# Performance work log

Hardware: AMD Instinct MI355X
Metric: run time of the kernel (lower is better)

Reference implementation:

```python
import jax, jax.numpy as jnp
import numpy as np

N_TOKENS = 4096
EMBED = 1024
ATTN = 64


def setup_inputs() -> dict:
    key = jax.random.key(0)
    k1, k2, k3, k4 = jax.random.split(key, 4)
    tokens = jax.random.normal(k1, (N_TOKENS, EMBED), dtype=jnp.float32)
    mask = jnp.ones((1, N_TOKENS), dtype=jnp.float32)
    W_Q = jax.random.uniform(k2, (EMBED, ATTN), dtype=jnp.float32)
    W_K = jax.random.uniform(k3, (EMBED, ATTN), dtype=jnp.float32)
    W_V = jax.random.uniform(k4, (EMBED, ATTN), dtype=jnp.float32)
    return {"tokens": tokens, "mask": mask, "W_Q": W_Q, "W_K": W_K, "W_V": W_V}


def reference(tokens, mask, W_Q, W_K, W_V):
    # Q, K, V: (n_tokens, attn)
    Q = tokens @ W_Q
    K = tokens @ W_K
    V = tokens @ W_V
    scale = jnp.sqrt(jnp.asarray(ATTN, dtype=tokens.dtype))
    # scores: (n_tokens, n_tokens); multiplicative mask then scale, as in source
    scores = (Q @ K.T) * mask
    attn = jax.nn.softmax(scores / scale, axis=1)
    return attn @ V
```

## Files before the change

kernel.cpp:

```cpp
#include <hip/hip_runtime.h>
#include <math.h>

#define NT 4096
#define EMB 1024
#define DH 64
#define PLANE (NT * DH)
#define NSPLIT 16
#define KPS (NT / NSPLIT)
#define KVB 128
#define KSPLIT 8
#define LOG2E 1.44269504088896f

typedef __attribute__((ext_vector_type(8))) short short8;
typedef __attribute__((ext_vector_type(16))) float f32x16;
typedef unsigned short u16;

union U8 { short8 s; uint4 u; unsigned short h[8]; unsigned int w[4]; };

static __device__ __forceinline__ unsigned short f2bf(float x) {
    union { float f; unsigned int u; } v; v.f = x;
    unsigned int r = v.u + 0x7fffu + ((v.u >> 16) & 1u);
    return (unsigned short)(r >> 16);
}
static __device__ __forceinline__ float bf2f(unsigned short h) {
    union { unsigned int u; float f; } v; v.u = ((unsigned int)h) << 16;
    return v.f;
}
static __device__ __forceinline__ unsigned int cvtpk(float a, float b) {
    unsigned int r;
    asm("v_cvt_pk_bf16_f32 %0, %1, %2" : "=v"(r) : "v"(a), "v"(b));
    return r;
}
static __device__ __forceinline__ void split2(float a, float b,
                                              unsigned int& h, unsigned int& lo) {
    h = cvtpk(a, b);
    union { unsigned int u; float f; } ua, ub;
    ua.u = h << 16;
    ub.u = h & 0xffff0000u;
    lo = cvtpk(a - ua.f, b - ub.f);
}

__global__ __launch_bounds__(256) void proj_mfma(
    const float* __restrict__ tokens,
    const float* __restrict__ wq, const float* __restrict__ wk,
    const float* __restrict__ wv,
    float* __restrict__ part)
{
    __shared__ u16 Th[128][64];
    __shared__ u16 Tl[128][64];
    __shared__ u16 Wh[96][64];
    __shared__ u16 Wl[96][64];

    const int t  = threadIdx.x;
    const int rb = blockIdx.x;
    const int cb = blockIdx.y;
    const int ks = blockIdx.z;
    const int w    = t >> 6;
    const int lane = t & 63;
    const int g    = lane >> 5;
    const int c    = lane & 31;
    const int rowbase = rb * 128;

    f32x16 acc[3];
#pragma unroll
    for (int ct = 0; ct < 3; ++ct)
#pragma unroll
        for (int i = 0; i < 16; ++i) acc[ct][i] = 0.f;

    for (int st = 0; st < 2; ++st) {
        const int kbase = ks * (EMB / KSPLIT) + st * 64;
        __syncthreads();
#pragma unroll
        for (int i = 0; i < 4; ++i) {
            int idx = t + 256 * i;
            int r = idx >> 3;
            int slot = idx & 7;
            const float* gp = tokens + (size_t)(rowbase + r) * EMB + kbase + slot * 8;
            float4 a = *(const float4*)gp;
            float4 b = *(const float4*)(gp + 4);
            uint4 H, L;
            split2(a.x, a.y, H.x, L.x);
            split2(a.z, a.w, H.y, L.y);
            split2(b.x, b.y, H.z, L.z);
            split2(b.z, b.w, H.w, L.w);
            int dst = (slot ^ (r & 7)) * 8;
            *(uint4*)&Th[r][dst] = H;
            *(uint4*)&Tl[r][dst] = L;
        }
#pragma unroll
        for (int i = 0; i < 3; ++i) {
            int idx = t + 256 * i;
            int col = idx >> 3;
            int slot = idx & 7;
            int colg = cb * 96 + col;
            const float* W = (colg < 64) ? wq : (colg < 128) ? wk : wv;
            const float* wp = W + (size_t)(kbase + slot * 8) * DH + (colg & 63);
            float x[8];
#pragma unroll
            for (int j = 0; j < 8; ++j) x[j] = wp[j * DH];
            uint4 H, L;
            split2(x[0], x[1], H.x, L.x);
            split2(x[2], x[3], H.y, L.y);
            split2(x[4], x[5], H.z, L.z);
            split2(x[6], x[7], H.w, L.w);
            int dst = (slot ^ (col & 7)) * 8;
            *(uint4*)&Wh[col][dst] = H;
            *(uint4*)&Wl[col][dst] = L;
        }
        __syncthreads();

#pragma unroll
        for (int kt = 0; kt < 4; ++kt) {
            int sA = kt * 2 + g;
            int offA = ((sA ^ (c & 7)) * 8);
            short8 ah = *(const short8*)&Th[w * 32 + c][offA];
            short8 al = *(const short8*)&Tl[w * 32 + c][offA];
#pragma unroll
            for (int ct = 0; ct < 3; ++ct) {
                short8 bh = *(const short8*)&Wh[ct * 32 + c][offA];
                short8 bl = *(const short8*)&Wl[ct * 32 + c][offA];
                acc[ct] = __builtin_amdgcn_mfma_f32_32x32x16_bf16(ah, bh, acc[ct], 0, 0, 0);
                acc[ct] = __builtin_amdgcn_mfma_f32_32x32x16_bf16(ah, bl, acc[ct], 0, 0, 0);
                acc[ct] = __builtin_amdgcn_mfma_f32_32x32x16_bf16(al, bh, acc[ct], 0, 0, 0);
            }
        }
    }

#pragma unroll
    for (int ct = 0; ct < 3; ++ct)
#pragma unroll
        for (int r = 0; r < 16; ++r) {
            int row_l = (r & 3) + 8 * (r >> 2) + 4 * g;
            part[((size_t)ks * NT + rowbase + w * 32 + row_l) * 192 + cb * 96 + ct * 32 + c]
                = acc[ct][r];
        }
}

__global__ __launch_bounds__(256) void merge_conv(
    const float* __restrict__ part, const float* __restrict__ mask,
    u16* __restrict__ Qhg, u16* __restrict__ Qlg,
    u16* __restrict__ Khg, u16* __restrict__ Klg, u16* __restrict__ Vbg)
{
    int tid = blockIdx.x * 256 + threadIdx.x;
    int row = tid / 24;
    int c8  = tid % 24;
    int colbase = c8 * 8;

    float v[8];
#pragma unroll
    for (int i = 0; i < 8; ++i) v[i] = 0.f;
#pragma unroll
    for (int s = 0; s < KSPLIT; ++s) {
        const float* p = part + ((size_t)s * NT + row) * 192 + colbase;
        float4 a = *(const float4*)p;
        float4 b = *(const float4*)(p + 4);
        v[0] += a.x; v[1] += a.y; v[2] += a.z; v[3] += a.w;
        v[4] += b.x; v[5] += b.y; v[6] += b.z; v[7] += b.w;
    }

    int plane = colbase >> 6;
    int pc = colbase & 63;
    size_t o = (size_t)row * DH + pc;
    if (plane == 0) {
        uint4 H, L;
        split2(v[0], v[1], H.x, L.x);
        split2(v[2], v[3], H.y, L.y);
        split2(v[4], v[5], H.z, L.z);
        split2(v[6], v[7], H.w, L.w);
        *(uint4*)&Qhg[o] = H;
        *(uint4*)&Qlg[o] = L;
    } else if (plane == 1) {
        float mk = mask[row] * 0.125f * LOG2E;
        uint4 H, L;
        split2(v[0] * mk, v[1] * mk, H.x, L.x);
        split2(v[2] * mk, v[3] * mk, H.y, L.y);
        split2(v[4] * mk, v[5] * mk, H.z, L.z);
        split2(v[6] * mk, v[7] * mk, H.w, L.w);
        *(uint4*)&Khg[o] = H;
        *(uint4*)&Klg[o] = L;
    } else {
        uint4 H;
        H.x = cvtpk(v[0], v[1]);
        H.y = cvtpk(v[2], v[3]);
        H.z = cvtpk(v[4], v[5]);
        H.w = cvtpk(v[6], v[7]);
        *(uint4*)&Vbg[o] = H;
    }
}

__global__ __launch_bounds__(256, 2) void attn_mfma(
    const u16* __restrict__ Qhg, const u16* __restrict__ Qlg,
    const u16* __restrict__ Khg, const u16* __restrict__ Klg,
    const u16* __restrict__ Vbg,
    u16* __restrict__ opart, float* __restrict__ mlbuf)
{
    __shared__ u16 Kh[128][64];
    __shared__ u16 Kl[128][64];
    __shared__ unsigned int V2[64][64];

    const int t    = threadIdx.x;
    const int qb   = blockIdx.x;
    const int sp   = blockIdx.y;
    const int wq   = t >> 6;
    const int lane = t & 63;
    const int g    = lane >> 5;
    const int c    = lane & 31;
    const int qrow = qb * 128 + wq * 32 + c;

    short8 qh[4], ql[4];
#pragma unroll
    for (int kt = 0; kt < 4; ++kt) {
        size_t o = (size_t)qrow * DH + kt * 16 + g * 8;
        U8 H, L;
        H.u = *(const uint4*)&Qhg[o];
        L.u = *(const uint4*)&Qlg[o];
        qh[kt] = H.s;
        ql[kt] = L.s;
    }

    f32x16 oa[2];
#pragma unroll
    for (int i = 0; i < 16; ++i) { oa[0][i] = 0.f; oa[1][i] = 0.f; }
    float m = -INFINITY, l = 0.f;

    for (int cb = 0; cb < KPS / KVB; ++cb) {
        const int kv = sp * KPS + cb * KVB;
        __syncthreads();
#pragma unroll
        for (int it = 0; it < 4; ++it) {
            int idx = it * 256 + t;
            int j = idx >> 3, gr = idx & 7;
            int colp = (gr * 8) ^ ((j & 7) * 8);
            *(uint4*)&Kh[j][colp] = *(const uint4*)&Khg[(size_t)(kv + j) * DH + gr * 8];
            *(uint4*)&Kl[j][colp] = *(const uint4*)&Klg[(size_t)(kv + j) * DH + gr * 8];
        }
#pragma unroll
        for (int it = 0; it < 2; ++it) {
            int idx = it * 256 + t;
            int a2 = idx >> 3, dg = idx & 7;
            uint4 r0 = *(const uint4*)&Vbg[(size_t)(kv + a2 * 2) * DH + dg * 8];
            uint4 r1 = *(const uint4*)&Vbg[(size_t)(kv + a2 * 2 + 1) * DH + dg * 8];
            const unsigned int* p0 = (const unsigned int*)&r0;
            const unsigned int* p1 = (const unsigned int*)&r1;
            unsigned int wv_[8];
#pragma unroll
            for (int i = 0; i < 4; ++i) {
                wv_[2 * i]     = (p0[i] & 0xFFFFu) | (p1[i] << 16);
                wv_[2 * i + 1] = (p0[i] >> 16)     | (p1[i] & 0xFFFF0000u);
            }
            int colp = (dg * 8) ^ ((a2 & 7) * 8);
            *(uint4*)&V2[a2][colp]     = *(uint4*)&wv_[0];
            *(uint4*)&V2[a2][colp + 4] = *(uint4*)&wv_[4];
        }
        __syncthreads();

        f32x16 st[4];
#pragma unroll
        for (int jt = 0; jt < 4; ++jt)
#pragma unroll
            for (int i = 0; i < 16; ++i) st[jt][i] = 0.f;
#pragma unroll
        for (int kt = 0; kt < 4; ++kt) {
            int colp = ((kt * 2 + g) * 8) ^ ((c & 7) * 8);
#pragma unroll
            for (int jt = 0; jt < 4; ++jt) {
                short8 kh = *(const short8*)&Kh[jt * 32 + c][colp];
                short8 kl = *(const short8*)&Kl[jt * 32 + c][colp];
                st[jt] = __builtin_amdgcn_mfma_f32_32x32x16_bf16(kh, qh[kt], st[jt], 0, 0, 0);
                st[jt] = __builtin_amdgcn_mfma_f32_32x32x16_bf16(kh, ql[kt], st[jt], 0, 0, 0);
                st[jt] = __builtin_amdgcn_mfma_f32_32x32x16_bf16(kl, qh[kt], st[jt], 0, 0, 0);
            }
        }

        float p[64];
        float pm = -INFINITY;
#pragma unroll
        for (int jt = 0; jt < 4; ++jt)
#pragma unroll
            for (int r = 0; r < 16; ++r) pm = fmaxf(pm, st[jt][r]);
        pm = fmaxf(pm, __shfl_xor(pm, 32));
        float mn = fmaxf(m, pm);
        float f  = exp2f(m - mn);
        float rs = 0.f;
#pragma unroll
        for (int jt = 0; jt < 4; ++jt)
#pragma unroll
            for (int r = 0; r < 16; ++r) {
                p[jt * 16 + r] = exp2f(st[jt][r] - mn);
                rs += p[jt * 16 + r];
            }
        rs += __shfl_xor(rs, 32);
        l = l * f + rs;
        m = mn;

        short8 pa[8];
#pragma unroll
        for (int jt = 0; jt < 4; ++jt) {
            const float* pp = &p[jt * 16];
            unsigned int A1 = cvtpk(pp[0], pp[1]),   B1 = cvtpk(pp[4], pp[5]);
            unsigned int A2 = cvtpk(pp[2], pp[3]),   B2 = cvtpk(pp[6], pp[7]);
            unsigned int A3 = cvtpk(pp[8], pp[9]),   B3 = cvtpk(pp[12], pp[13]);
            unsigned int A4 = cvtpk(pp[10], pp[11]), B4 = cvtpk(pp[14], pp[15]);
            unsigned int xA1 = (unsigned int)__shfl_xor((int)A1, 32);
            unsigned int xB1 = (unsigned int)__shfl_xor((int)B1, 32);
            unsigned int xA2 = (unsigned int)__shfl_xor((int)A2, 32);
            unsigned int xB2 = (unsigned int)__shfl_xor((int)B2, 32);
            unsigned int xA3 = (unsigned int)__shfl_xor((int)A3, 32);
            unsigned int xB3 = (unsigned int)__shfl_xor((int)B3, 32);
            unsigned int xA4 = (unsigned int)__shfl_xor((int)A4, 32);
            unsigned int xB4 = (unsigned int)__shfl_xor((int)B4, 32);
            U8 f0, f1;
            f0.w[0] = g ? xB1 : A1;
            f0.w[1] = g ? xB2 : A2;
            f0.w[2] = g ? B1  : xA1;
            f0.w[3] = g ? B2  : xA2;
            f1.w[0] = g ? xB3 : A3;
            f1.w[1] = g ? xB4 : A4;
            f1.w[2] = g ? B3  : xA3;
            f1.w[3] = g ? B4  : xA4;
            pa[jt * 2]     = f0.s;
            pa[jt * 2 + 1] = f1.s;
        }

#pragma unroll
        for (int r = 0; r < 16; ++r) {
            float fr = __shfl(f, (r & 3) + 8 * (r >> 2) + 4 * g);
            oa[0][r] *= fr;
            oa[1][r] *= fr;
        }

#pragma unroll
        for (int dt = 0; dt < 2; ++dt) {
#pragma unroll
            for (int ksl = 0; ksl < 8; ++ksl) {
                U8 bf;
#pragma unroll
                for (int pq = 0; pq < 4; ++pq) {
                    int j2 = ksl * 8 + g * 4 + pq;
                    int col = (dt * 32 + c) ^ ((j2 & 7) * 8);
                    bf.w[pq] = V2[j2][col];
                }
                oa[dt] = __builtin_amdgcn_mfma_f32_32x32x16_bf16(pa[ksl], bf.s, oa[dt], 0, 0, 0);
            }
        }
    }

    float inv = 1.f / l;
#pragma unroll
    for (int r = 0; r < 16; ++r) {
        int crow = (r & 3) + 8 * (r >> 2) + 4 * g;
        float li = __shfl(inv, crow);
        int row = qb * 128 + wq * 32 + crow;
        size_t o = ((size_t)sp * NT + row) * DH + c;
        opart[o]      = f2bf(oa[0][r] * li);
        opart[o + 32] = f2bf(oa[1][r] * li);
    }
    if (lane < 32) {
        int row = qb * 128 + wq * 32 + lane;
        mlbuf[((size_t)sp * NT + row) * 2 + 0] = m;
        mlbuf[((size_t)sp * NT + row) * 2 + 1] = l;
    }
}

__global__ __launch_bounds__(256) void merge_kernel(
    const u16* __restrict__ opart, const float* __restrict__ mlbuf,
    float* __restrict__ out)
{
    int idx = (blockIdx.x * 256 + threadIdx.x) * 4;
    int row = idx >> 6;
    int d0  = idx & 63;

    float mv[NSPLIT], lv[NSPLIT];
    float mstar = -INFINITY;
#pragma unroll
    for (int s = 0; s < NSPLIT; ++s) {
        mv[s] = mlbuf[((size_t)s * NT + row) * 2 + 0];
        lv[s] = mlbuf[((size_t)s * NT + row) * 2 + 1];
        mstar = fmaxf(mstar, mv[s]);
    }
    float denom = 0.f;
    float ax = 0.f, ay = 0.f, az = 0.f, aw = 0.f;
#pragma unroll
    for (int s = 0; s < NSPLIT; ++s) {
        float w = lv[s] * exp2f(mv[s] - mstar);
        denom += w;
        uint2 ov = *(const uint2*)&opart[((size_t)s * NT + row) * DH + d0];
        ax += w * bf2f((u16)(ov.x & 0xFFFFu));
        ay += w * bf2f((u16)(ov.x >> 16));
        az += w * bf2f((u16)(ov.y & 0xFFFFu));
        aw += w * bf2f((u16)(ov.y >> 16));
    }
    float inv = 1.f / denom;
    *(float4*)&out[idx] = make_float4(ax * inv, ay * inv, az * inv, aw * inv);
}

extern "C" void kernel_launch(void* const* d_in, const int* in_sizes, int n_in,
                              void* d_out, int out_size, void* d_ws, size_t ws_size,
                              hipStream_t stream) {
    const float* tokens = (const float*)d_in[0];
    const float* mask   = (const float*)d_in[1];
    const float* wq     = (const float*)d_in[2];
    const float* wk     = (const float*)d_in[3];
    const float* wv     = (const float*)d_in[4];
    char*  wsb = (char*)d_ws;
    float* out = (float*)d_out;

    u16* Qhg  = (u16*)wsb;
    u16* Qlg  = Qhg + PLANE;
    u16* Khg  = Qlg + PLANE;
    u16* Klg  = Khg + PLANE;
    u16* Vbg  = Klg + PLANE;
    float* part  = (float*)(wsb + (size_t)4 * 1024 * 1024);
    u16*   opart = (u16*)(wsb + (size_t)4 * 1024 * 1024);
    float* mlbuf = (float*)(wsb + (size_t)28 * 1024 * 1024);

    hipLaunchKernelGGL(proj_mfma, dim3(32, 2, KSPLIT), dim3(256), 0, stream,
                       tokens, wq, wk, wv, part);
    hipLaunchKernelGGL(merge_conv, dim3(384), dim3(256), 0, stream,
                       part, mask, Qhg, Qlg, Khg, Klg, Vbg);
    hipLaunchKernelGGL(attn_mfma, dim3(NT / 128, NSPLIT), dim3(256), 0, stream,
                       Qhg, Qlg, Khg, Klg, Vbg, opart, mlbuf);
    hipLaunchKernelGGL(merge_kernel, dim3(256), dim3(256), 0, stream,
                       opart, mlbuf, out);
}
```

Measured before the change: 48.50 us.

## Pre-split weights in a prep kernel and keep token fragments in registers

Adds a small prep_w kernel that converts W_Q/W_K/W_V into transposed bf16 hi/lo planes once per call. proj_mfma then copies those planes straight into LDS with vector loads, instead of doing strided fp32 gathers and splits in every block. Each lane now loads its own token row slice straight into registers and splits it there, so the token LDS staging and the two-stage loop with its barriers go away. The cost is an extra kernel launch, an extra workspace round-trip for the weights, and higher register pressure under the new two-blocks-per-SM launch bound.

```diff
diff --git a/kernel.cpp b/kernel.cpp
--- a/kernel.cpp
+++ b/kernel.cpp
@@ -40,16 +40,36 @@
     lo = cvtpk(a - ua.f, b - ub.f);
 }
 
-__global__ __launch_bounds__(256) void proj_mfma(
-    const float* __restrict__ tokens,
+__global__ __launch_bounds__(256) void prep_w(
     const float* __restrict__ wq, const float* __restrict__ wk,
     const float* __restrict__ wv,
+    u16* __restrict__ WtSh, u16* __restrict__ WtSl)
+{
+    int tid = blockIdx.x * 256 + threadIdx.x;
+    int col = tid >> 7;
+    int ch  = tid & 127;
+    const float* W = (col < 64) ? wq : (col < 128) ? wk : wv;
+    int wcol = col & 63;
+    int k0 = ch * 8;
+    float x[8];
+#pragma unroll
+    for (int i = 0; i < 8; ++i) x[i] = W[(size_t)(k0 + i) * DH + wcol];
+    uint4 H, L;
+    split2(x[0], x[1], H.x, L.x);
+    split2(x[2], x[3], H.y, L.y);
+    split2(x[4], x[5], H.z, L.z);
+    split2(x[6], x[7], H.w, L.w);
+    *(uint4*)&WtSh[(size_t)col * EMB + k0] = H;
+    *(uint4*)&WtSl[(size_t)col * EMB + k0] = L;
+}
+
+__global__ __launch_bounds__(256, 2) void proj_mfma(
+    const float* __restrict__ tokens,
+    const u16* __restrict__ WtSh, const u16* __restrict__ WtSl,
     float* __restrict__ part)
 {
-    __shared__ u16 Th[128][64];
-    __shared__ u16 Tl[128][64];
-    __shared__ u16 Wh[96][64];
-    __shared__ u16 Wl[96][64];
+    __shared__ u16 Wh[96][128];
+    __shared__ u16 Wl[96][128];
 
     const int t  = threadIdx.x;
     const int rb = blockIdx.x;
@@ -60,6 +80,39 @@
     const int g    = lane >> 5;
     const int c    = lane & 31;
     const int rowbase = rb * 128;
+    const int kbase = ks * (EMB / KSPLIT);
+
+    const float* trow = tokens + (size_t)(rowbase + w * 32 + c) * EMB + kbase;
+    float4 ta[8], tb[8];
+#pragma unroll
+    for (int kt = 0; kt < 8; ++kt) {
+        ta[kt] = *(const float4*)(trow + kt * 16 + g * 8);
+        tb[kt] = *(const float4*)(trow + kt * 16 + g * 8 + 4);
+    }
+
+#pragma unroll
+    for (int i = 0; i < 6; ++i) {
+        int idx = t + 256 * i;
+        int col = idx >> 4;
+        int slot = idx & 15;
+        size_t gi = (size_t)(cb * 96 + col) * EMB + kbase + slot * 8;
+        int dst = (slot ^ (col & 7)) * 8;
+        *(uint4*)&Wh[col][dst] = *(const uint4*)&WtSh[gi];
+        *(uint4*)&Wl[col][dst] = *(const uint4*)&WtSl[gi];
+    }
+    __syncthreads();
+
+    short8 ah[8], al[8];
+#pragma unroll
+    for (int kt = 0; kt < 8; ++kt) {
+        U8 H, L;
+        split2(ta[kt].x, ta[kt].y, H.w[0], L.w[0]);
+        split2(ta[kt].z, ta[kt].w, H.w[1], L.w[1]);
+        split2(tb[kt].x, tb[kt].y, H.w[2], L.w[2]);
+        split2(tb[kt].z, tb[kt].w, H.w[3], L.w[3]);
+        ah[kt] = H.s;
+        al[kt] = L.s;
+    }
 
     f32x16 acc[3];
 #pragma unroll
@@ -67,62 +120,16 @@
 #pragma unroll
         for (int i = 0; i < 16; ++i) acc[ct][i] = 0.f;
 
-    for (int st = 0; st < 2; ++st) {
-        const int kbase = ks * (EMB / KSPLIT) + st * 64;
-        __syncthreads();
-#pragma unroll
-        for (int i = 0; i < 4; ++i) {
-            int idx = t + 256 * i;
-            int r = idx >> 3;
-            int slot = idx & 7;
-            const float* gp = tokens + (size_t)(rowbase + r) * EMB + kbase + slot * 8;
-            float4 a = *(const float4*)gp;
-            float4 b = *(const float4*)(gp + 4);
-            uint4 H, L;
-            split2(a.x, a.y, H.x, L.x);
-            split2(a.z, a.w, H.y, L.y);
-            split2(b.x, b.y, H.z, L.z);
-            split2(b.z, b.w, H.w, L.w);
-            int dst = (slot ^ (r & 7)) * 8;
-            *(uint4*)&Th[r][dst] = H;
-            *(uint4*)&Tl[r][dst] = L;
-        }
-#pragma unroll
-        for (int i = 0; i < 3; ++i) {
-            int idx = t + 256 * i;
-            int col = idx >> 3;
-            int slot = idx & 7;
-            int colg = cb * 96 + col;
-            const float* W = (colg < 64) ? wq : (colg < 128) ? wk : wv;
-            const float* wp = W + (size_t)(kbase + slot * 8) * DH + (colg & 63);
-            float x[8];
-#pragma unroll
-            for (int j = 0; j < 8; ++j) x[j] = wp[j * DH];
-            uint4 H, L;
-            split2(x[0], x[1], H.x, L.x);
-            split2(x[2], x[3], H.y, L.y);
-            split2(x[4], x[5], H.z, L.z);
-            split2(x[6], x[7], H.w, L.w);
-            int dst = (slot ^ (col & 7)) * 8;
-            *(uint4*)&Wh[col][dst] = H;
-            *(uint4*)&Wl[col][dst] = L;
-        }
-        __syncthreads();
-
-#pragma unroll
-        for (int kt = 0; kt < 4; ++kt) {
-            int sA = kt * 2 + g;
-            int offA = ((sA ^ (c & 7)) * 8);
-            short8 ah = *(const short8*)&Th[w * 32 + c][offA];
-            short8 al = *(const short8*)&Tl[w * 32 + c][offA];
-#pragma unroll
-            for (int ct = 0; ct < 3; ++ct) {
-                short8 bh = *(const short8*)&Wh[ct * 32 + c][offA];
-                short8 bl = *(const short8*)&Wl[ct * 32 + c][offA];
-                acc[ct] = __builtin_amdgcn_mfma_f32_32x32x16_bf16(ah, bh, acc[ct], 0, 0, 0);
-                acc[ct] = __builtin_amdgcn_mfma_f32_32x32x16_bf16(ah, bl, acc[ct], 0, 0, 0);
-                acc[ct] = __builtin_amdgcn_mfma_f32_32x32x16_bf16(al, bh, acc[ct], 0, 0, 0);
-            }
+#pragma unroll
+    for (int kt = 0; kt < 8; ++kt) {
+        int offA = (((kt * 2 + g) ^ (c & 7)) * 8);
+#pragma unroll
+        for (int ct = 0; ct < 3; ++ct) {
+            short8 bh = *(const short8*)&Wh[ct * 32 + c][offA];
+            short8 bl = *(const short8*)&Wl[ct * 32 + c][offA];
+            acc[ct] = __builtin_amdgcn_mfma_f32_32x32x16_bf16(ah[kt], bh, acc[ct], 0, 0, 0);
+            acc[ct] = __builtin_amdgcn_mfma_f32_32x32x16_bf16(ah[kt], bl, acc[ct], 0, 0, 0);
+            acc[ct] = __builtin_amdgcn_mfma_f32_32x32x16_bf16(al[kt], bh, acc[ct], 0, 0, 0);
         }
     }
 
@@ -405,7 +412,9 @@
     char*  wsb = (char*)d_ws;
     float* out = (float*)d_out;
 
-    u16* Qhg  = (u16*)wsb;
+    u16* WtSh = (u16*)wsb;
+    u16* WtSl = WtSh + 192 * EMB;
+    u16* Qhg  = WtSl + 192 * EMB;
     u16* Qlg  = Qhg + PLANE;
     u16* Khg  = Qlg + PLANE;
     u16* Klg  = Khg + PLANE;
@@ -414,8 +423,10 @@
     u16*   opart = (u16*)(wsb + (size_t)4 * 1024 * 1024);
     float* mlbuf = (float*)(wsb + (size_t)28 * 1024 * 1024);
 
+    hipLaunchKernelGGL(prep_w, dim3(96), dim3(256), 0, stream,
+                       wq, wk, wv, WtSh, WtSl);
     hipLaunchKernelGGL(proj_mfma, dim3(32, 2, KSPLIT), dim3(256), 0, stream,
-                       tokens, wq, wk, wv, part);
+                       tokens, WtSh, WtSl, part);
     hipLaunchKernelGGL(merge_conv, dim3(384), dim3(256), 0, stream,
                        part, mask, Qhg, Qlg, Khg, Klg, Vbg);
     hipLaunchKernelGGL(attn_mfma, dim3(NT / 128, NSPLIT), dim3(256), 0, stream,
```

After: 49.04 us. No clear change (+1.1%).
